# Performance work log

Measured on AMD Instinct MI355X. Metric: run time of the kernel, lower is better.

The kernel has to match this reference:

```python
import jax, jax.numpy as jnp
import numpy as np
import math

CAPACITY_FACTOR = 1.0

def setup_inputs() -> dict:
    key = jax.random.key(0)
    k1, k2 = jax.random.split(key)
    x = jax.random.normal(k1, (8192, 2048), dtype=jnp.float32)
    wg = jax.random.normal(k2, (64, 2048), dtype=jnp.float32) * (1.0 / np.sqrt(2048))
    return {"x": x, "wg": wg}

def reference(x, wg):
    # logits = Linear(model_dim, num_experts, bias=False)(x)
    logits = jnp.einsum('sd,ed->se', x, wg)
    gates = jax.nn.softmax(logits, axis=1)  # [s, e]
    s, e = gates.shape
    capacity = math.ceil(s / e * CAPACITY_FACTOR)  # static
    indices1_s = jnp.argmax(gates, axis=1)  # [s]
    mask1 = jax.nn.one_hot(indices1_s, e, dtype=jnp.int32)  # [s, e]
    locations1 = jnp.cumsum(mask1, axis=0) - 1  # position within each expert queue
    # aux load-balancing loss
    me = jnp.mean(gates, axis=0)
    ce = jnp.mean(mask1.astype(gates.dtype), axis=0)
    l_aux = jnp.mean(me * ce) * (e * e)
    # drop tokens over capacity
    mask1 = mask1 * (locations1 < capacity).astype(jnp.int32)
    locations1_s = jnp.sum(locations1 * mask1, axis=1)  # [s] int
    mask1_float = mask1.astype(gates.dtype)
    gates1_s = jnp.sum(gates * mask1_float, axis=1)  # 'se,se->s'
    gates1 = gates1_s[:, None] * mask1_float         # 's,se->se'
    locations1_sc = jax.nn.one_hot(locations1_s, capacity, dtype=gates.dtype)  # [s, c]
    combine_weights = gates1[:, :, None] * locations1_sc[:, None, :]  # 'se,sc->sec'
    dispatch_mask = combine_weights.astype(bool)
    return l_aux, combine_weights, dispatch_mask
```

## Files before the change

### kernel.cpp

```cpp
#include <hip/hip_runtime.h>
#include <cstdint>
#include <cstddef>


#define S_TOK 8192
#define NEXP 64
#define DIM 2048
#define CAP 128
#define TOK_PER_BLK 32
#define KC 32
#define COMB_ELEMS ((size_t)S_TOK * NEXP * CAP)

__global__ __launch_bounds__(256) void gate_kernel(
    const float* __restrict__ x, const float* __restrict__ wg,
    int* __restrict__ idx_out, float* __restrict__ gate_out,
    float* __restrict__ gsum)
{
    __shared__ float xs[KC][TOK_PER_BLK];
    __shared__ float wsh[KC][NEXP];
    __shared__ float sme[NEXP];

    const int tid = threadIdx.x;
    const int tok0 = blockIdx.x * TOK_PER_BLK;
    const int ty = tid >> 5;
    const int tx = tid & 31;
    const int t0 = ty * 4;
    const int e0 = tx * 2;

    if (tid < NEXP) sme[tid] = 0.0f;

    float acc[4][2];
#pragma unroll
    for (int i = 0; i < 4; ++i) { acc[i][0] = 0.0f; acc[i][1] = 0.0f; }

    const int xt = tid >> 3;
    const int xk = (tid & 7) * 4;
    const float* xrow = x + (size_t)(tok0 + xt) * DIM + xk;
    const int we0 = tid >> 3;
    const float* wrow0 = wg + (size_t)we0 * DIM + xk;
    const float* wrow1 = wrow0 + (size_t)32 * DIM;

    float4 xv  = *(const float4*)(xrow);
    float4 wv0 = *(const float4*)(wrow0);
    float4 wv1 = *(const float4*)(wrow1);

    for (int kc = 0; kc < DIM; kc += KC) {
        __syncthreads();
        xs[xk + 0][xt] = xv.x; xs[xk + 1][xt] = xv.y;
        xs[xk + 2][xt] = xv.z; xs[xk + 3][xt] = xv.w;
        wsh[xk + 0][we0] = wv0.x; wsh[xk + 1][we0] = wv0.y;
        wsh[xk + 2][we0] = wv0.z; wsh[xk + 3][we0] = wv0.w;
        wsh[xk + 0][we0 + 32] = wv1.x; wsh[xk + 1][we0 + 32] = wv1.y;
        wsh[xk + 2][we0 + 32] = wv1.z; wsh[xk + 3][we0 + 32] = wv1.w;
        __syncthreads();
        if (kc + KC < DIM) {
            xv  = *(const float4*)(xrow + kc + KC);
            wv0 = *(const float4*)(wrow0 + kc + KC);
            wv1 = *(const float4*)(wrow1 + kc + KC);
        }
#pragma unroll
        for (int k = 0; k < KC; ++k) {
            float4 xa = *(const float4*)&xs[k][t0];
            float2 wb = *(const float2*)&wsh[k][e0];
            acc[0][0] += xa.x * wb.x; acc[0][1] += xa.x * wb.y;
            acc[1][0] += xa.y * wb.x; acc[1][1] += xa.y * wb.y;
            acc[2][0] += xa.z * wb.x; acc[2][1] += xa.z * wb.y;
            acc[3][0] += xa.w * wb.x; acc[3][1] += xa.w * wb.y;
        }
    }

    float gm0 = 0.0f, gm1 = 0.0f;
#pragma unroll
    for (int i = 0; i < 4; ++i) {
        float l0 = acc[i][0], l1 = acc[i][1];
        float v; int ix;
        if (l1 > l0) { v = l1; ix = e0 + 1; } else { v = l0; ix = e0; }
#pragma unroll
        for (int off = 16; off; off >>= 1) {
            float ov = __shfl_xor(v, off, 32);
            int   oi = __shfl_xor(ix, off, 32);
            if (ov > v || (ov == v && oi < ix)) { v = ov; ix = oi; }
        }
        float z0 = __expf(l0 - v), z1 = __expf(l1 - v);
        float zs = z0 + z1;
#pragma unroll
        for (int off = 16; off; off >>= 1) zs += __shfl_xor(zs, off, 32);
        float inv = 1.0f / zs;
        gm0 += z0 * inv; gm1 += z1 * inv;
        if (tx == 0) {
            int tok = tok0 + t0 + i;
            idx_out[tok]  = ix;
            gate_out[tok] = inv;
        }
    }
    atomicAdd(&sme[e0], gm0);
    atomicAdd(&sme[e0 + 1], gm1);
    __syncthreads();
    if (tid < NEXP) atomicAdd(&gsum[tid], sme[tid]);
}

__global__ __launch_bounds__(1024) void scan_scatter(
    const int* __restrict__ idx, const float* __restrict__ gate,
    const float* __restrict__ gsum, float* __restrict__ out)
{
    __shared__ int wavecnt[16][NEXP];
    __shared__ int basecnt[NEXP];
    const int tid  = threadIdx.x;
    const int lane = tid & 63;
    const int wv   = tid >> 6;

    if (tid < NEXP) basecnt[tid] = 0;
    __syncthreads();

    for (int it = 0; it < S_TOK / 1024; ++it) {
        int tok = it * 1024 + tid;
        int e = idx[tok];
        unsigned long long m = ~0ull, lm = ~0ull;
#pragma unroll
        for (int b = 0; b < 6; ++b) {
            unsigned long long bal = __ballot((e >> b) & 1);
            m  &= ((e >> b) & 1)    ? bal : ~bal;
            lm &= ((lane >> b) & 1) ? bal : ~bal;
        }
        int rank = __popcll(m & ((1ull << lane) - 1ull));
        wavecnt[wv][lane] = __popcll(lm);
        __syncthreads();
        int off = 0;
        for (int w = 0; w < wv; ++w) off += wavecnt[w][e];
        int loc = basecnt[e] + off + rank;
        if (loc < CAP) {
            size_t base = 1 + (size_t)tok * (NEXP * CAP) + (size_t)e * CAP + loc;
            out[base] = gate[tok];
            out[base + COMB_ELEMS] = 1.0f;
        }
        __syncthreads();
        if (tid < NEXP) {
            int tot = 0;
#pragma unroll
            for (int w = 0; w < 16; ++w) tot += wavecnt[w][tid];
            basecnt[tid] += tot;
        }
        __syncthreads();
    }

    if (tid < NEXP) {
        float p = gsum[tid] * (float)basecnt[tid];
#pragma unroll
        for (int off = 32; off; off >>= 1) p += __shfl_xor(p, off, 64);
        if (tid == 0) out[0] = p * 9.5367431640625e-07f;
    }
}

extern "C" void kernel_launch(void* const* d_in, const int* in_sizes, int n_in,
                              void* d_out, int out_size, void* d_ws, size_t ws_size,
                              hipStream_t stream) {
    const float* x  = (const float*)d_in[0];
    const float* wg = (const float*)d_in[1];
    float* out = (float*)d_out;

    int*   idx  = (int*)d_ws;
    float* gate = (float*)((char*)d_ws + 32768);
    float* gsum = (float*)((char*)d_ws + 65536);

    hipMemsetAsync(d_out, 0, (size_t)out_size * sizeof(float), stream);
    hipMemsetAsync(gsum, 0, NEXP * sizeof(float), stream);

    gate_kernel<<<S_TOK / TOK_PER_BLK, 256, 0, stream>>>(x, wg, idx, gate, gsum);
    scan_scatter<<<1, 1024, 0, stream>>>(idx, gate, gsum, out);
}
```

Before: 634.5 us.

## Split gating GEMM over K slices and fuse zero-fill with scatter writer

The single gate kernel becomes a split-K logits kernel with larger 128-token tiles and 8x4 register blocking, plus a separate reduce kernel that sums the partials and does softmax/argmax. The scan now only computes locations. A new writer kernel produces the whole output in one pass with float4 stores, writing either zero or the selected value, so the full-buffer memset and the scattered writes go away. The costs are an extra partial-logits buffer round trip, two more kernel launches, and index arithmetic for every output element.

```diff
diff --git a/kernel.cpp b/kernel.cpp
--- a/kernel.cpp
+++ b/kernel.cpp
@@ -7,21 +7,109 @@
 #define NEXP 64
 #define DIM 2048
 #define CAP 128
-#define TOK_PER_BLK 32
+#define COMB_ELEMS ((size_t)S_TOK * NEXP * CAP)
+#define OUT_ELEMS (1 + 2 * COMB_ELEMS)
+
+#define TOK_TILE 128
+#define NSLICE 4
+#define KSLICE (DIM / NSLICE)
 #define KC 32
-#define COMB_ELEMS ((size_t)S_TOK * NEXP * CAP)
-
-__global__ __launch_bounds__(256) void gate_kernel(
+
+__global__ __launch_bounds__(256) void logits_kernel(
     const float* __restrict__ x, const float* __restrict__ wg,
+    float* __restrict__ P)
+{
+    __shared__ float xs[KC][132];
+    __shared__ float wsh[KC][68];
+
+    const int tid  = threadIdx.x;
+    const int tile  = blockIdx.x >> 2;
+    const int slice = blockIdx.x & 3;
+    const int tok0 = tile * TOK_TILE;
+    const int k0   = slice * KSLICE;
+
+    const int tt = tid >> 4;
+    const int te = tid & 15;
+
+    float acc[8][4];
+#pragma unroll
+    for (int i = 0; i < 8; ++i)
+#pragma unroll
+        for (int j = 0; j < 4; ++j) acc[i][j] = 0.0f;
+
+    const int we  = tid & 63;
+    const int wkq = tid >> 6;
+
+    float4 xv[4], wv[2];
+#pragma unroll
+    for (int r = 0; r < 4; ++r) {
+        int idx = tid + 256 * r;
+        int t = idx >> 3, kq = idx & 7;
+        xv[r] = *(const float4*)(x + (size_t)(tok0 + t) * DIM + k0 + 4 * kq);
+    }
+    wv[0] = *(const float4*)(wg + (size_t)we * DIM + k0 + 4 * wkq);
+    wv[1] = *(const float4*)(wg + (size_t)we * DIM + k0 + 4 * (wkq + 4));
+
+    for (int kc = 0; kc < KSLICE; kc += KC) {
+        __syncthreads();
+#pragma unroll
+        for (int r = 0; r < 4; ++r) {
+            int idx = tid + 256 * r;
+            int t = idx >> 3, k4 = (idx & 7) * 4;
+            xs[k4 + 0][t] = xv[r].x; xs[k4 + 1][t] = xv[r].y;
+            xs[k4 + 2][t] = xv[r].z; xs[k4 + 3][t] = xv[r].w;
+        }
+        {
+            int k4 = 4 * wkq;
+            wsh[k4 + 0][we] = wv[0].x; wsh[k4 + 1][we] = wv[0].y;
+            wsh[k4 + 2][we] = wv[0].z; wsh[k4 + 3][we] = wv[0].w;
+            int k4b = k4 + 16;
+            wsh[k4b + 0][we] = wv[1].x; wsh[k4b + 1][we] = wv[1].y;
+            wsh[k4b + 2][we] = wv[1].z; wsh[k4b + 3][we] = wv[1].w;
+        }
+        __syncthreads();
+        if (kc + KC < KSLICE) {
+#pragma unroll
+            for (int r = 0; r < 4; ++r) {
+                int idx = tid + 256 * r;
+                int t = idx >> 3, kq = idx & 7;
+                xv[r] = *(const float4*)(x + (size_t)(tok0 + t) * DIM + k0 + kc + KC + 4 * kq);
+            }
+            wv[0] = *(const float4*)(wg + (size_t)we * DIM + k0 + kc + KC + 4 * wkq);
+            wv[1] = *(const float4*)(wg + (size_t)we * DIM + k0 + kc + KC + 4 * (wkq + 4));
+        }
+#pragma unroll 8
+        for (int k = 0; k < KC; ++k) {
+            float4 a0 = *(const float4*)&xs[k][8 * tt];
+            float4 a1 = *(const float4*)&xs[k][8 * tt + 4];
+            float4 b  = *(const float4*)&wsh[k][4 * te];
+            const float* ap0 = &a0.x; const float* ap1 = &a1.x; const float* bp = &b.x;
+#pragma unroll
+            for (int i = 0; i < 4; ++i)
+#pragma unroll
+                for (int j = 0; j < 4; ++j) {
+                    acc[i][j]     += ap0[i] * bp[j];
+                    acc[i + 4][j] += ap1[i] * bp[j];
+                }
+        }
+    }
+
+#pragma unroll
+    for (int i = 0; i < 8; ++i) {
+        size_t off = ((size_t)slice * S_TOK + tok0 + 8 * tt + i) * NEXP + 4 * te;
+        float4 v = { acc[i][0], acc[i][1], acc[i][2], acc[i][3] };
+        *(float4*)(P + off) = v;
+    }
+}
+
+__global__ __launch_bounds__(256) void reduce_kernel(
+    const float* __restrict__ P,
     int* __restrict__ idx_out, float* __restrict__ gate_out,
     float* __restrict__ gsum)
 {
-    __shared__ float xs[KC][TOK_PER_BLK];
-    __shared__ float wsh[KC][NEXP];
     __shared__ float sme[NEXP];
-
     const int tid = threadIdx.x;
-    const int tok0 = blockIdx.x * TOK_PER_BLK;
+    const int tok0 = blockIdx.x * 32;
     const int ty = tid >> 5;
     const int tx = tid & 31;
     const int t0 = ty * 4;
@@ -29,50 +117,16 @@
 
     if (tid < NEXP) sme[tid] = 0.0f;
 
-    float acc[4][2];
-#pragma unroll
-    for (int i = 0; i < 4; ++i) { acc[i][0] = 0.0f; acc[i][1] = 0.0f; }
-
-    const int xt = tid >> 3;
-    const int xk = (tid & 7) * 4;
-    const float* xrow = x + (size_t)(tok0 + xt) * DIM + xk;
-    const int we0 = tid >> 3;
-    const float* wrow0 = wg + (size_t)we0 * DIM + xk;
-    const float* wrow1 = wrow0 + (size_t)32 * DIM;
-
-    float4 xv  = *(const float4*)(xrow);
-    float4 wv0 = *(const float4*)(wrow0);
-    float4 wv1 = *(const float4*)(wrow1);
-
-    for (int kc = 0; kc < DIM; kc += KC) {
-        __syncthreads();
-        xs[xk + 0][xt] = xv.x; xs[xk + 1][xt] = xv.y;
-        xs[xk + 2][xt] = xv.z; xs[xk + 3][xt] = xv.w;
-        wsh[xk + 0][we0] = wv0.x; wsh[xk + 1][we0] = wv0.y;
-        wsh[xk + 2][we0] = wv0.z; wsh[xk + 3][we0] = wv0.w;
-        wsh[xk + 0][we0 + 32] = wv1.x; wsh[xk + 1][we0 + 32] = wv1.y;
-        wsh[xk + 2][we0 + 32] = wv1.z; wsh[xk + 3][we0 + 32] = wv1.w;
-        __syncthreads();
-        if (kc + KC < DIM) {
-            xv  = *(const float4*)(xrow + kc + KC);
-            wv0 = *(const float4*)(wrow0 + kc + KC);
-            wv1 = *(const float4*)(wrow1 + kc + KC);
-        }
-#pragma unroll
-        for (int k = 0; k < KC; ++k) {
-            float4 xa = *(const float4*)&xs[k][t0];
-            float2 wb = *(const float2*)&wsh[k][e0];
-            acc[0][0] += xa.x * wb.x; acc[0][1] += xa.x * wb.y;
-            acc[1][0] += xa.y * wb.x; acc[1][1] += xa.y * wb.y;
-            acc[2][0] += xa.z * wb.x; acc[2][1] += xa.z * wb.y;
-            acc[3][0] += xa.w * wb.x; acc[3][1] += xa.w * wb.y;
-        }
-    }
-
     float gm0 = 0.0f, gm1 = 0.0f;
 #pragma unroll
     for (int i = 0; i < 4; ++i) {
-        float l0 = acc[i][0], l1 = acc[i][1];
+        int tok = tok0 + t0 + i;
+        float l0 = 0.0f, l1 = 0.0f;
+#pragma unroll
+        for (int s = 0; s < NSLICE; ++s) {
+            float2 p = *(const float2*)&P[((size_t)s * S_TOK + tok) * NEXP + e0];
+            l0 += p.x; l1 += p.y;
+        }
         float v; int ix;
         if (l1 > l0) { v = l1; ix = e0 + 1; } else { v = l0; ix = e0; }
 #pragma unroll
@@ -88,7 +142,6 @@
         float inv = 1.0f / zs;
         gm0 += z0 * inv; gm1 += z1 * inv;
         if (tx == 0) {
-            int tok = tok0 + t0 + i;
             idx_out[tok]  = ix;
             gate_out[tok] = inv;
         }
@@ -99,9 +152,9 @@
     if (tid < NEXP) atomicAdd(&gsum[tid], sme[tid]);
 }
 
-__global__ __launch_bounds__(1024) void scan_scatter(
-    const int* __restrict__ idx, const float* __restrict__ gate,
-    const float* __restrict__ gsum, float* __restrict__ out)
+__global__ __launch_bounds__(1024) void scan_kernel(
+    const int* __restrict__ idx, const float* __restrict__ gsum,
+    int* __restrict__ loc_out, float* __restrict__ laux_out)
 {
     __shared__ int wavecnt[16][NEXP];
     __shared__ int basecnt[NEXP];
@@ -127,12 +180,7 @@
         __syncthreads();
         int off = 0;
         for (int w = 0; w < wv; ++w) off += wavecnt[w][e];
-        int loc = basecnt[e] + off + rank;
-        if (loc < CAP) {
-            size_t base = 1 + (size_t)tok * (NEXP * CAP) + (size_t)e * CAP + loc;
-            out[base] = gate[tok];
-            out[base + COMB_ELEMS] = 1.0f;
-        }
+        loc_out[tok] = basecnt[e] + off + rank;
         __syncthreads();
         if (tid < NEXP) {
             int tot = 0;
@@ -147,7 +195,39 @@
         float p = gsum[tid] * (float)basecnt[tid];
 #pragma unroll
         for (int off = 32; off; off >>= 1) p += __shfl_xor(p, off, 64);
-        if (tid == 0) out[0] = p * 9.5367431640625e-07f;
+        if (tid == 0) laux_out[0] = p * 9.5367431640625e-07f;
+    }
+}
+
+__global__ __launch_bounds__(256) void writer_kernel(
+    const int* __restrict__ idx, const float* __restrict__ gate,
+    const int* __restrict__ loc, const float* __restrict__ laux,
+    float* __restrict__ out)
+{
+    size_t base = (size_t)blockIdx.x * 1024 + threadIdx.x;
+#pragma unroll
+    for (int r = 0; r < 4; ++r) {
+        size_t j = base + 256 * (size_t)r;
+        size_t i0 = j * 4;
+        float4 v = { 0.0f, 0.0f, 0.0f, 0.0f };
+        float* vp = &v.x;
+#pragma unroll
+        for (int jj = 0; jj < 4; ++jj) {
+            size_t i = i0 + jj;
+            if (i == 0) { vp[jj] = laux[0]; continue; }
+            size_t q = i - 1;
+            bool sel = q >= COMB_ELEMS;
+            size_t p = sel ? q - COMB_ELEMS : q;
+            int t = (int)(p >> 13);
+            int rr = (int)(p & 8191);
+            int e = rr >> 7, c = rr & 127;
+            if (e == idx[t] && c == loc[t])
+                vp[jj] = sel ? 1.0f : gate[t];
+        }
+        *(float4*)(out + i0) = v;
+    }
+    if (blockIdx.x == 0 && threadIdx.x == 0) {
+        out[OUT_ELEMS - 1] = (idx[S_TOK - 1] == 63 && loc[S_TOK - 1] == 127) ? 1.0f : 0.0f;
     }
 }
 
@@ -161,10 +241,14 @@
     int*   idx  = (int*)d_ws;
     float* gate = (float*)((char*)d_ws + 32768);
     float* gsum = (float*)((char*)d_ws + 65536);
-
-    hipMemsetAsync(d_out, 0, (size_t)out_size * sizeof(float), stream);
+    float* laux = (float*)((char*)d_ws + 65792);
+    int*   loc  = (int*)((char*)d_ws + 66560);
+    float* P    = (float*)((char*)d_ws + 131072);
+
     hipMemsetAsync(gsum, 0, NEXP * sizeof(float), stream);
 
-    gate_kernel<<<S_TOK / TOK_PER_BLK, 256, 0, stream>>>(x, wg, idx, gate, gsum);
-    scan_scatter<<<1, 1024, 0, stream>>>(idx, gate, gsum, out);
-}
+    logits_kernel<<<(S_TOK / TOK_TILE) * NSLICE, 256, 0, stream>>>(x, wg, P);
+    reduce_kernel<<<S_TOK / 32, 256, 0, stream>>>(P, idx, gate, gsum);
+    scan_kernel<<<1, 1024, 0, stream>>>(idx, gsum, loc, laux);
+    writer_kernel<<<32768, 256, 0, stream>>>(idx, gate, loc, laux, out);
+}
```

After: 619.7 us. -2.3%, faster.
